# Kernel tuning notes

Measured on AMD Instinct MI355X. Metric: run time of the kernel, lower is better.

## Reference

```python
import jax, jax.numpy as jnp
import numpy as np

N_NODES = 50000
N_EDGES = 1600000
N_GRAPHS = 512
IN_DIM = 64
HID = 128
OUT_DIM = 10


def setup_inputs() -> dict:
    key = jax.random.key(0)
    ks = jax.random.split(key, 12)
    x = jax.random.normal(ks[0], (N_NODES, IN_DIM), dtype=jnp.float32)
    edge_index = jax.random.randint(ks[1], (2, N_EDGES), 0, N_NODES, dtype=jnp.int64)
    batch = jnp.sort(jax.random.randint(ks[2], (N_NODES,), 0, N_GRAPHS, dtype=jnp.int64))
    edge_attr = jax.random.uniform(ks[3], (N_EDGES,), dtype=jnp.float32)
    # glorot-ish init for weights
    def lin(k, fan_in, fan_out):
        s = (6.0 / (fan_in + fan_out)) ** 0.5
        return jax.random.uniform(k, (fan_in, fan_out), minval=-s, maxval=s, dtype=jnp.float32)
    return {
        "x": x, "edge_index": edge_index, "batch": batch, "edge_attr": edge_attr,
        "W1": lin(ks[4], IN_DIM, HID), "b1": jnp.zeros((HID,), jnp.float32),
        "W2": lin(ks[5], HID, HID), "b2": jnp.zeros((HID,), jnp.float32),
        "Wm1": lin(ks[6], HID, HID), "bm1": jnp.zeros((HID,), jnp.float32),
        "Wm2": lin(ks[7], HID, OUT_DIM), "bm2": jnp.zeros((OUT_DIM,), jnp.float32),
    }


def _gcn_conv(x, edge_index, edge_weight, W, b, num_nodes):
    """PyG GCNConv: add self-loops, symmetric norm with edge weights, x@W, scatter-add, +bias."""
    loop = jnp.arange(num_nodes, dtype=edge_index.dtype)
    src = jnp.concatenate([edge_index[0], loop])
    dst = jnp.concatenate([edge_index[1], loop])
    ew = jnp.concatenate([edge_weight, jnp.ones((num_nodes,), edge_weight.dtype)])
    deg = jax.ops.segment_sum(ew, dst, num_segments=num_nodes)  # [N]
    dinv = jnp.where(deg > 0, jax.lax.rsqrt(jnp.where(deg > 0, deg, 1.0)), 0.0)
    norm = dinv[src] * ew * dinv[dst]  # [E+N]
    h = x @ W  # [N, F_out]
    msg = h[src] * norm[:, None]  # gather + scale
    out = jax.ops.segment_sum(msg, dst, num_segments=num_nodes)
    return out + b


def reference(x, edge_index, batch, edge_attr, W1, b1, W2, b2, Wm1, bm1, Wm2, bm2):
    n = x.shape[0]
    h = _gcn_conv(x, edge_index, edge_attr, W1, b1, n)
    h = jax.nn.relu(h)  # dropout = identity in eval mode
    h = _gcn_conv(h, edge_index, edge_attr, W2, b2, n)
    h = jax.nn.relu(h)
    pooled = jax.ops.segment_sum(h, batch, num_segments=N_GRAPHS)  # global_add_pool
    z = jax.nn.relu(pooled @ Wm1 + bm1)
    return z @ Wm2 + bm2  # [num_graphs, out_dim]
```

## Files before the change

kernel.cpp:

```cpp
#include <hip/hip_runtime.h>
#include <hip/hip_bf16.h>
#include <hip/hip_fp16.h>
#include <cstdint>

#define HIDC 128
#define FIXSCALE 4194304.0f
#define FIXINV   (1.0f / 4194304.0f)
#define MAXDEG 80

#define BKT_SHIFT 7
#define BKT_NODES 128
#define BKT_CAP   6144
#define BIN_TILE  4096
#define BIN_THREADS 512

typedef _Float16 half8 __attribute__((ext_vector_type(8)));
typedef float float4v __attribute__((ext_vector_type(4)));

__global__ __launch_bounds__(256) void prep_kernel(
        const float* __restrict__ W1, const float* __restrict__ W2,
        _Float16* __restrict__ W1t, _Float16* __restrict__ W2t,
        unsigned int* __restrict__ tails, int nbkt) {
    int i = blockIdx.x * 256 + threadIdx.x;
    if (i < 16384) { int k = i >> 7, n = i & 127; W2t[n * 128 + k] = (_Float16)W2[i]; }
    if (i < 8192)  { int k = i >> 7, n = i & 127; W1t[n * 64 + k]  = (_Float16)W1[i]; }
    if (i < nbkt) tails[i] = 0u;
}

__global__ __launch_bounds__(BIN_THREADS) void bin_kernel(
        const int* __restrict__ ei, const float* __restrict__ ea,
        unsigned long long* __restrict__ buck, unsigned int* __restrict__ tails,
        int E, int nbkt) {
    __shared__ unsigned long long rec[BIN_TILE];
    __shared__ unsigned int cnt[BIN_THREADS];
    __shared__ unsigned int startx[BIN_THREADS];
    __shared__ unsigned int cur[BIN_THREADS];
    __shared__ unsigned int gbase[BIN_THREADS];
    int t = threadIdx.x;
    int base = blockIdx.x * BIN_TILE;
    int total = E - base; if (total > BIN_TILE) total = BIN_TILE;

    cnt[t] = 0;
    __syncthreads();

    unsigned int lo[8], dv[8];
#pragma unroll
    for (int j = 0; j < 8; ++j) {
        int e = base + j * BIN_THREADS + t;
        if (e < E) {
            int s = ei[e]; int d = ei[E + e]; float w = ea[e];
            lo[j] = (unsigned int)s |
                    ((unsigned int)__half_as_ushort(__float2half_rn(w)) << 16);
            dv[j] = (unsigned int)d;
            atomicAdd(&cnt[dv[j] >> BKT_SHIFT], 1u);
        } else dv[j] = 0xffffffffu;
    }
    __syncthreads();

    startx[t] = cnt[t];
    __syncthreads();
    for (int off = 1; off < BIN_THREADS; off <<= 1) {
        unsigned int add = (t >= off) ? startx[t - off] : 0u;
        __syncthreads();
        startx[t] += add;
        __syncthreads();
    }
    unsigned int excl = startx[t] - cnt[t];
    startx[t] = excl;
    cur[t] = excl;
    if (t < nbkt) gbase[t] = atomicAdd(&tails[t], cnt[t]);
    __syncthreads();

#pragma unroll
    for (int j = 0; j < 8; ++j) {
        if (dv[j] != 0xffffffffu) {
            unsigned int p = atomicAdd(&cur[dv[j] >> BKT_SHIFT], 1u);
            rec[p] = ((unsigned long long)dv[j] << 32) | (unsigned long long)lo[j];
        }
    }
    __syncthreads();

    for (int i = t; i < total; i += BIN_THREADS) {
        unsigned long long r = rec[i];
        unsigned int b = ((unsigned int)(r >> 32)) >> BKT_SHIFT;
        unsigned int idx = gbase[b] + ((unsigned int)i - startx[b]);
        if (idx < BKT_CAP) buck[(size_t)b * BKT_CAP + idx] = r;
    }
}

__global__ __launch_bounds__(256) void fill_kernel(
        const unsigned long long* __restrict__ buck,
        const unsigned int* __restrict__ tails,
        unsigned long long* __restrict__ degcnt,
        unsigned int* __restrict__ padcsr, int n_nodes) {
    __shared__ unsigned long long deg[BKT_NODES];
    int b = blockIdx.x, t = threadIdx.x;
    if (t < BKT_NODES) deg[t] = 0ull;
    __syncthreads();
    int cnt_b = (int)tails[b]; if (cnt_b > BKT_CAP) cnt_b = BKT_CAP;
    const unsigned long long* rb = buck + (size_t)b * BKT_CAP;
    int nodeBase = b << BKT_SHIFT;
    for (int i = t; i < cnt_b; i += 256) {
        unsigned long long r = rb[i];
        unsigned int lo = (unsigned int)r;
        unsigned int dl = ((unsigned int)(r >> 32)) & (BKT_NODES - 1);
        float w = __half2float(__ushort_as_half((unsigned short)(lo >> 16)));
        unsigned int fx = (unsigned int)(w * FIXSCALE + 0.5f);
        unsigned long long old =
            atomicAdd(&deg[dl], (1ull << 32) | (unsigned long long)fx);
        unsigned int rank = (unsigned int)(old >> 32);
        if (rank < MAXDEG)
            padcsr[(size_t)(nodeBase + dl) * MAXDEG + rank] = lo;
    }
    __syncthreads();
    if (t < BKT_NODES) {
        int node = nodeBase + t;
        if (node < n_nodes) degcnt[node] = deg[t];
    }
}

__global__ __launch_bounds__(256) void gemm1_mfma_kernel(
        const float* __restrict__ X,
        const _Float16* __restrict__ W1t,
        const unsigned long long* __restrict__ degcnt,
        __half* __restrict__ out, int n_nodes) {
    int wave = threadIdx.x >> 6, lane = threadIdx.x & 63;
    int nodeBase = (blockIdx.x * 4 + wave) * 16;
    if (nodeBase >= n_nodes) return;
    int mrow = lane & 15, quad = lane >> 4;

    int anode = nodeBase + mrow; if (anode >= n_nodes) anode = n_nodes - 1;
    const float* Arow = X + (size_t)anode * 64 + quad * 8;
    half8 a[2];
#pragma unroll
    for (int q = 0; q < 2; ++q) {
        float4v f0 = *(const float4v*)(Arow + q * 32);
        float4v f1 = *(const float4v*)(Arow + q * 32 + 4);
        half8 hv;
#pragma unroll
        for (int j = 0; j < 4; ++j) { hv[j] = (_Float16)f0[j]; hv[j + 4] = (_Float16)f1[j]; }
        a[q] = hv;
    }

    float4v acc[8];
#pragma unroll
    for (int nt = 0; nt < 8; ++nt) acc[nt] = (float4v)(0.f);
#pragma unroll
    for (int nt = 0; nt < 8; ++nt) {
        const _Float16* Brow = W1t + (size_t)(nt * 16 + mrow) * 64 + quad * 8;
#pragma unroll
        for (int q = 0; q < 2; ++q) {
            half8 b = *(const half8*)(Brow + q * 32);
            acc[nt] = __builtin_amdgcn_mfma_f32_16x16x32_f16(a[q], b, acc[nt], 0, 0, 0);
        }
    }
#pragma unroll
    for (int r = 0; r < 4; ++r) {
        int node = nodeBase + quad * 4 + r;
        if (node < n_nodes) {
            unsigned long long v = degcnt[node];
            float di = rsqrtf(1.0f + (float)(unsigned int)(v & 0xffffffffull) * FIXINV);
#pragma unroll
            for (int nt = 0; nt < 8; ++nt)
                out[(size_t)node * 128 + nt * 16 + mrow] = __float2half(acc[nt][r] * di);
        }
    }
}

__global__ __launch_bounds__(256) void gemm2_mfma_kernel(
        const __half* __restrict__ A,
        const _Float16* __restrict__ W2t,
        const unsigned long long* __restrict__ degcnt,
        __half* __restrict__ out, int n_nodes) {
    int wave = threadIdx.x >> 6, lane = threadIdx.x & 63;
    int nodeBase = (blockIdx.x * 4 + wave) * 16;
    if (nodeBase >= n_nodes) return;
    int mrow = lane & 15, quad = lane >> 4;

    int anode = nodeBase + mrow; if (anode >= n_nodes) anode = n_nodes - 1;
    const _Float16* Arow = (const _Float16*)A + (size_t)anode * 128 + quad * 8;
    half8 a[4];
#pragma unroll
    for (int q = 0; q < 4; ++q) a[q] = *(const half8*)(Arow + q * 32);

    float4v acc[8];
#pragma unroll
    for (int nt = 0; nt < 8; ++nt) acc[nt] = (float4v)(0.f);
#pragma unroll
    for (int nt = 0; nt < 8; ++nt) {
        const _Float16* Brow = W2t + (size_t)(nt * 16 + mrow) * 128 + quad * 8;
#pragma unroll
        for (int q = 0; q < 4; ++q) {
            half8 b = *(const half8*)(Brow + q * 32);
            acc[nt] = __builtin_amdgcn_mfma_f32_16x16x32_f16(a[q], b, acc[nt], 0, 0, 0);
        }
    }
#pragma unroll
    for (int r = 0; r < 4; ++r) {
        int node = nodeBase + quad * 4 + r;
        if (node < n_nodes) {
            unsigned long long v = degcnt[node];
            float di = rsqrtf(1.0f + (float)(unsigned int)(v & 0xffffffffull) * FIXINV);
#pragma unroll
            for (int nt = 0; nt < 8; ++nt)
                out[(size_t)node * 128 + nt * 16 + mrow] = __float2half(acc[nt][r] * di);
        }
    }
}

__global__ __launch_bounds__(256) void agg_kernel(const __half* __restrict__ h,
                                                  const unsigned long long* __restrict__ degcnt,
                                                  const unsigned int* __restrict__ padcsr,
                                                  const float* __restrict__ bias,
                                                  __half* __restrict__ out, int n_nodes) {
    int wave = threadIdx.x >> 6;
    int lane = threadIdx.x & 63;
    int node = blockIdx.x * 4 + wave;
    if (node >= n_nodes) return;
    unsigned long long v = degcnt[node];
    int cnt = (int)(v >> 32);
    if (cnt > MAXDEG) cnt = MAXDEG;
    float di = rsqrtf(1.0f + (float)(unsigned int)(v & 0xffffffffull) * FIXINV);
    const unsigned int* row = padcsr + (size_t)node * MAXDEG;
    float a0 = 0.f, a1 = 0.f;
    int e = 0;
    for (; e + 16 <= cnt; e += 16) {
        unsigned int p[16];
#pragma unroll
        for (int j = 0; j < 16; ++j) p[j] = row[e + j];
        __half2 vv[16];
#pragma unroll
        for (int j = 0; j < 16; ++j)
            vv[j] = *(reinterpret_cast<const __half2*>(h + (p[j] & 0xffffu) * HIDC) + lane);
#pragma unroll
        for (int j = 0; j < 16; ++j) {
            float c = __half2float(__ushort_as_half((unsigned short)(p[j] >> 16)));
            float2 f = __half22float2(vv[j]);
            a0 = fmaf(c, f.x, a0); a1 = fmaf(c, f.y, a1);
        }
    }
    for (; e + 4 <= cnt; e += 4) {
        unsigned int p[4];
#pragma unroll
        for (int j = 0; j < 4; ++j) p[j] = row[e + j];
        __half2 vv[4];
#pragma unroll
        for (int j = 0; j < 4; ++j)
            vv[j] = *(reinterpret_cast<const __half2*>(h + (p[j] & 0xffffu) * HIDC) + lane);
#pragma unroll
        for (int j = 0; j < 4; ++j) {
            float c = __half2float(__ushort_as_half((unsigned short)(p[j] >> 16)));
            float2 f = __half22float2(vv[j]);
            a0 = fmaf(c, f.x, a0); a1 = fmaf(c, f.y, a1);
        }
    }
    for (; e < cnt; ++e) {
        unsigned int p = row[e];
        float c = __half2float(__ushort_as_half((unsigned short)(p >> 16)));
        float2 f = __half22float2(*(reinterpret_cast<const __half2*>(h + (p & 0xffffu) * HIDC) + lane));
        a0 = fmaf(c, f.x, a0); a1 = fmaf(c, f.y, a1);
    }
    float2 fn = __half22float2(*(reinterpret_cast<const __half2*>(h + (size_t)node * HIDC) + lane));
    a0 = di * (a0 + fn.x);
    a1 = di * (a1 + fn.y);
    float2 bb = *(reinterpret_cast<const float2*>(bias) + lane);
    a0 = fmaxf(a0 + bb.x, 0.f);
    a1 = fmaxf(a1 + bb.y, 0.f);
    *(reinterpret_cast<__half2*>(out + (size_t)node * HIDC) + lane) =
        __floats2half2_rn(a0, a1);
}

__global__ __launch_bounds__(128) void pool_mlp_kernel(const __half* __restrict__ h,
                                                       const int* __restrict__ batch,
                                                       const float* __restrict__ Wm1,
                                                       const float* __restrict__ bm1,
                                                       const float* __restrict__ Wm2,
                                                       const float* __restrict__ bm2,
                                                       float* __restrict__ out,
                                                       int n_nodes, int out_dim) {
    int g = blockIdx.x;
    int t = threadIdx.x;
    __shared__ int sb[2];
    if (t < 2) {
        int target = g + t;
        int lo = 0, hi = n_nodes;
        while (lo < hi) { int mid = (lo + hi) >> 1; if (batch[mid] < target) lo = mid + 1; else hi = mid; }
        sb[t] = lo;
    }
    __syncthreads();
    int beg = sb[0], end = sb[1];
    float p = 0.f;
    for (int i = beg; i < end; ++i) p += __half2float(h[(size_t)i * 128 + t]);
    __shared__ float row[128];
    __shared__ float z[128];
    row[t] = p;
    __syncthreads();
    float acc = bm1[t];
#pragma unroll 8
    for (int k = 0; k < 128; ++k) acc += row[k] * Wm1[k * 128 + t];
    z[t] = fmaxf(acc, 0.f);
    __syncthreads();
    if (t < out_dim) {
        float o = bm2[t];
#pragma unroll 8
        for (int k = 0; k < 128; ++k) o += z[k] * Wm2[k * out_dim + t];
        out[g * out_dim + t] = o;
    }
}

extern "C" void kernel_launch(void* const* d_in, const int* in_sizes, int n_in,
                              void* d_out, int out_size, void* d_ws, size_t ws_size,
                              hipStream_t stream) {
    const float* x   = (const float*)d_in[0];
    const int*   ei  = (const int*)d_in[1];
    const int*   bat = (const int*)d_in[2];
    const float* ea  = (const float*)d_in[3];
    const float* W1  = (const float*)d_in[4];
    const float* b1  = (const float*)d_in[5];
    const float* W2  = (const float*)d_in[6];
    const float* b2  = (const float*)d_in[7];
    const float* Wm1 = (const float*)d_in[8];
    const float* bm1 = (const float*)d_in[9];
    const float* Wm2 = (const float*)d_in[10];
    const float* bm2 = (const float*)d_in[11];
    float* out = (float*)d_out;

    const int N = in_sizes[2];
    const int E = in_sizes[1] / 2;
    const int N_GRAPHS = 512;
    const int OUT_DIM = out_size / N_GRAPHS;

    char* ws = (char*)d_ws;
    size_t off = 0;
    auto alloc = [&](size_t bytes) { char* p = ws + off; off += (bytes + 255) & ~size_t(255); return p; };
    __half* bufA    = (__half*)alloc((size_t)N * HIDC * 2);
    __half* bufR    = (__half*)alloc((size_t)N * HIDC * 2);
    unsigned int* padcsr = (unsigned int*)alloc((size_t)N * MAXDEG * 4);
    unsigned long long* degcnt = (unsigned long long*)alloc((size_t)N * 8);
    _Float16* W2t   = (_Float16*)alloc(128 * 128 * 2);
    _Float16* W1t   = (_Float16*)alloc(128 * 64 * 2);
    unsigned int* tails = (unsigned int*)alloc(BIN_THREADS * 4);

    unsigned long long* buck = (unsigned long long*)bufA;
    int nbkt = (N + BKT_NODES - 1) >> BKT_SHIFT;

    prep_kernel<<<64, 256, 0, stream>>>(W1, W2, W1t, W2t, tails, nbkt);
    int binBlocks = (E + BIN_TILE - 1) / BIN_TILE;
    bin_kernel<<<binBlocks, BIN_THREADS, 0, stream>>>(ei, ea, buck, tails, E, nbkt);
    fill_kernel<<<nbkt, 256, 0, stream>>>(buck, tails, degcnt, padcsr, N);
    gemm1_mfma_kernel<<<(N + 63) / 64, 256, 0, stream>>>(x, W1t, degcnt, bufA, N);
    agg_kernel<<<(N + 3) / 4, 256, 0, stream>>>(bufA, degcnt, padcsr, b1, bufR, N);
    gemm2_mfma_kernel<<<(N + 63) / 64, 256, 0, stream>>>(bufR, W2t, degcnt, bufA, N);
    agg_kernel<<<(N + 3) / 4, 256, 0, stream>>>(bufA, degcnt, padcsr, b2, bufR, N);
    pool_mlp_kernel<<<N_GRAPHS, 128, 0, stream>>>(bufR, bat, Wm1, bm1, Wm2, bm2, out, N, OUT_DIM);
}
```

Before: 303.4 us.

## Reorder GCN layers to aggregate before transform and shrink bucket records

Layer 1 now aggregates the 64-wide pre-scaled input features (computed in fill_kernel) before the GEMM, and layer 2 aggregates before multiplying by W2. Bias and ReLU are folded into the GEMM epilogues. The first aggregation gathers half as much data, and the second GEMM no longer needs the degree scaling. Bucket records are split into a 4-byte payload plus a 1-byte local destination with a smaller capacity, the bin scan uses wave shuffles, and the pool kernel uses 256 threads. The risks are fp16 rounding in a different order and possible bucket overflow at the reduced capacity.

New measurement: 278.3 us. -8.3%, faster.

```diff
diff --git a/kernel.cpp b/kernel.cpp
--- a/kernel.cpp
+++ b/kernel.cpp
@@ -10,7 +10,7 @@
 
 #define BKT_SHIFT 7
 #define BKT_NODES 128
-#define BKT_CAP   6144
+#define BKT_CAP   4608
 #define BIN_TILE  4096
 #define BIN_THREADS 512
 
@@ -29,13 +29,14 @@
 
 __global__ __launch_bounds__(BIN_THREADS) void bin_kernel(
         const int* __restrict__ ei, const float* __restrict__ ea,
-        unsigned long long* __restrict__ buck, unsigned int* __restrict__ tails,
-        int E, int nbkt) {
+        unsigned int* __restrict__ buck_lo, unsigned char* __restrict__ buck_dl,
+        unsigned int* __restrict__ tails, int E, int nbkt) {
     __shared__ unsigned long long rec[BIN_TILE];
     __shared__ unsigned int cnt[BIN_THREADS];
     __shared__ unsigned int startx[BIN_THREADS];
     __shared__ unsigned int cur[BIN_THREADS];
     __shared__ unsigned int gbase[BIN_THREADS];
+    __shared__ unsigned int wtot[BIN_THREADS / 64];
     int t = threadIdx.x;
     int base = blockIdx.x * BIN_TILE;
     int total = E - base; if (total > BIN_TILE) total = BIN_TILE;
@@ -57,18 +58,22 @@
     }
     __syncthreads();
 
-    startx[t] = cnt[t];
-    __syncthreads();
-    for (int off = 1; off < BIN_THREADS; off <<= 1) {
-        unsigned int add = (t >= off) ? startx[t - off] : 0u;
-        __syncthreads();
-        startx[t] += add;
-        __syncthreads();
-    }
-    unsigned int excl = startx[t] - cnt[t];
+    unsigned int c = cnt[t];
+    unsigned int sc = c;
+#pragma unroll
+    for (int off = 1; off < 64; off <<= 1) {
+        unsigned int v = __shfl_up(sc, off);
+        if ((t & 63) >= off) sc += v;
+    }
+    if ((t & 63) == 63) wtot[t >> 6] = sc;
+    __syncthreads();
+    unsigned int wbase = 0;
+    int w = t >> 6;
+    for (int i = 0; i < w; ++i) wbase += wtot[i];
+    unsigned int excl = sc + wbase - c;
     startx[t] = excl;
     cur[t] = excl;
-    if (t < nbkt) gbase[t] = atomicAdd(&tails[t], cnt[t]);
+    if (t < nbkt) gbase[t] = atomicAdd(&tails[t], c);
     __syncthreads();
 
 #pragma unroll
@@ -82,28 +87,35 @@
 
     for (int i = t; i < total; i += BIN_THREADS) {
         unsigned long long r = rec[i];
-        unsigned int b = ((unsigned int)(r >> 32)) >> BKT_SHIFT;
+        unsigned int hi = (unsigned int)(r >> 32);
+        unsigned int b = hi >> BKT_SHIFT;
         unsigned int idx = gbase[b] + ((unsigned int)i - startx[b]);
-        if (idx < BKT_CAP) buck[(size_t)b * BKT_CAP + idx] = r;
+        if (idx < BKT_CAP) {
+            buck_lo[b * BKT_CAP + idx] = (unsigned int)r;
+            buck_dl[b * BKT_CAP + idx] = (unsigned char)(hi & (BKT_NODES - 1));
+        }
     }
 }
 
 __global__ __launch_bounds__(256) void fill_kernel(
-        const unsigned long long* __restrict__ buck,
+        const unsigned int* __restrict__ buck_lo,
+        const unsigned char* __restrict__ buck_dl,
         const unsigned int* __restrict__ tails,
+        const float* __restrict__ x,
         unsigned long long* __restrict__ degcnt,
-        unsigned int* __restrict__ padcsr, int n_nodes) {
+        unsigned int* __restrict__ padcsr,
+        _Float16* __restrict__ xt, int n_nodes) {
     __shared__ unsigned long long deg[BKT_NODES];
+    __shared__ float sdinv[BKT_NODES];
     int b = blockIdx.x, t = threadIdx.x;
     if (t < BKT_NODES) deg[t] = 0ull;
     __syncthreads();
     int cnt_b = (int)tails[b]; if (cnt_b > BKT_CAP) cnt_b = BKT_CAP;
-    const unsigned long long* rb = buck + (size_t)b * BKT_CAP;
+    unsigned int boff = (unsigned int)b * BKT_CAP;
     int nodeBase = b << BKT_SHIFT;
     for (int i = t; i < cnt_b; i += 256) {
-        unsigned long long r = rb[i];
-        unsigned int lo = (unsigned int)r;
-        unsigned int dl = ((unsigned int)(r >> 32)) & (BKT_NODES - 1);
+        unsigned int lo = buck_lo[boff + i];
+        unsigned int dl = buck_dl[boff + i];
         float w = __half2float(__ushort_as_half((unsigned short)(lo >> 16)));
         unsigned int fx = (unsigned int)(w * FIXSCALE + 0.5f);
         unsigned long long old =
@@ -114,14 +126,85 @@
     }
     __syncthreads();
     if (t < BKT_NODES) {
+        unsigned long long dv = deg[t];
+        sdinv[t] = rsqrtf(1.0f + (float)(unsigned int)(dv & 0xffffffffull) * FIXINV);
         int node = nodeBase + t;
-        if (node < n_nodes) degcnt[node] = deg[t];
-    }
+        if (node < n_nodes) degcnt[node] = dv;
+    }
+    __syncthreads();
+    int d = t & 63, nl = t >> 6;
+    for (int nn = nl; nn < BKT_NODES; nn += 4) {
+        int node = nodeBase + nn;
+        if (node < n_nodes)
+            xt[(size_t)node * 64 + d] = (_Float16)(x[(size_t)node * 64 + d] * sdinv[nn]);
+    }
+}
+
+__global__ __launch_bounds__(256) void agg0_kernel(
+        const _Float16* __restrict__ xt,
+        const unsigned long long* __restrict__ degcnt,
+        const unsigned int* __restrict__ padcsr,
+        _Float16* __restrict__ g, int n_nodes) {
+    int wave = threadIdx.x >> 6, lane = threadIdx.x & 63;
+    int node = blockIdx.x * 4 + wave;
+    if (node >= n_nodes) return;
+    int half = lane >> 5, li = lane & 31;
+    unsigned long long v = degcnt[node];
+    int cnt = (int)(v >> 32); if (cnt > MAXDEG) cnt = MAXDEG;
+    float di = rsqrtf(1.0f + (float)(unsigned int)(v & 0xffffffffull) * FIXINV);
+    const unsigned int* row = padcsr + (size_t)node * MAXDEG;
+    const __half2* X = (const __half2*)xt;
+    float a0 = 0.f, a1 = 0.f;
+    int e = 0;
+    for (; e + 32 <= cnt; e += 32) {
+        unsigned int p[16];
+#pragma unroll
+        for (int j = 0; j < 16; ++j) p[j] = row[e + 2 * j + half];
+        __half2 vv[16];
+#pragma unroll
+        for (int j = 0; j < 16; ++j)
+            vv[j] = X[(p[j] & 0xffffu) * 32u + (unsigned)li];
+#pragma unroll
+        for (int j = 0; j < 16; ++j) {
+            float c = __half2float(__ushort_as_half((unsigned short)(p[j] >> 16)));
+            float2 f = __half22float2(vv[j]);
+            a0 = fmaf(c, f.x, a0); a1 = fmaf(c, f.y, a1);
+        }
+    }
+    if (e < cnt) {
+        int rem = cnt - e;
+        unsigned int p[16]; bool m[16];
+#pragma unroll
+        for (int j = 0; j < 16; ++j) {
+            int idx = 2 * j + half;
+            m[j] = idx < rem;
+            p[j] = m[j] ? row[e + idx] : 0u;
+        }
+        __half2 vv[16];
+#pragma unroll
+        for (int j = 0; j < 16; ++j)
+            vv[j] = X[(p[j] & 0xffffu) * 32u + (unsigned)li];
+#pragma unroll
+        for (int j = 0; j < 16; ++j) {
+            float c = m[j] ? __half2float(__ushort_as_half((unsigned short)(p[j] >> 16))) : 0.f;
+            float2 f = __half22float2(vv[j]);
+            a0 = fmaf(c, f.x, a0); a1 = fmaf(c, f.y, a1);
+        }
+    }
+    if (half == 0) {
+        float2 f = __half22float2(X[(unsigned)node * 32u + (unsigned)li]);
+        a0 += f.x; a1 += f.y;
+    }
+    a0 += __shfl_xor(a0, 32);
+    a1 += __shfl_xor(a1, 32);
+    if (half == 0)
+        *((__half2*)g + (unsigned)node * 32u + li) = __floats2half2_rn(di * a0, di * a1);
 }
 
 __global__ __launch_bounds__(256) void gemm1_mfma_kernel(
-        const float* __restrict__ X,
+        const _Float16* __restrict__ G,
         const _Float16* __restrict__ W1t,
+        const float* __restrict__ b1,
         const unsigned long long* __restrict__ degcnt,
         __half* __restrict__ out, int n_nodes) {
     int wave = threadIdx.x >> 6, lane = threadIdx.x & 63;
@@ -130,17 +213,10 @@
     int mrow = lane & 15, quad = lane >> 4;
 
     int anode = nodeBase + mrow; if (anode >= n_nodes) anode = n_nodes - 1;
-    const float* Arow = X + (size_t)anode * 64 + quad * 8;
+    const _Float16* Arow = G + (size_t)anode * 64 + quad * 8;
     half8 a[2];
-#pragma unroll
-    for (int q = 0; q < 2; ++q) {
-        float4v f0 = *(const float4v*)(Arow + q * 32);
-        float4v f1 = *(const float4v*)(Arow + q * 32 + 4);
-        half8 hv;
-#pragma unroll
-        for (int j = 0; j < 4; ++j) { hv[j] = (_Float16)f0[j]; hv[j + 4] = (_Float16)f1[j]; }
-        a[q] = hv;
-    }
+    a[0] = *(const half8*)(Arow);
+    a[1] = *(const half8*)(Arow + 32);
 
     float4v acc[8];
 #pragma unroll
@@ -161,58 +237,19 @@
             unsigned long long v = degcnt[node];
             float di = rsqrtf(1.0f + (float)(unsigned int)(v & 0xffffffffull) * FIXINV);
 #pragma unroll
-            for (int nt = 0; nt < 8; ++nt)
-                out[(size_t)node * 128 + nt * 16 + mrow] = __float2half(acc[nt][r] * di);
-        }
-    }
-}
-
-__global__ __launch_bounds__(256) void gemm2_mfma_kernel(
-        const __half* __restrict__ A,
-        const _Float16* __restrict__ W2t,
-        const unsigned long long* __restrict__ degcnt,
-        __half* __restrict__ out, int n_nodes) {
-    int wave = threadIdx.x >> 6, lane = threadIdx.x & 63;
-    int nodeBase = (blockIdx.x * 4 + wave) * 16;
-    if (nodeBase >= n_nodes) return;
-    int mrow = lane & 15, quad = lane >> 4;
-
-    int anode = nodeBase + mrow; if (anode >= n_nodes) anode = n_nodes - 1;
-    const _Float16* Arow = (const _Float16*)A + (size_t)anode * 128 + quad * 8;
-    half8 a[4];
-#pragma unroll
-    for (int q = 0; q < 4; ++q) a[q] = *(const half8*)(Arow + q * 32);
-
-    float4v acc[8];
-#pragma unroll
-    for (int nt = 0; nt < 8; ++nt) acc[nt] = (float4v)(0.f);
-#pragma unroll
-    for (int nt = 0; nt < 8; ++nt) {
-        const _Float16* Brow = W2t + (size_t)(nt * 16 + mrow) * 128 + quad * 8;
-#pragma unroll
-        for (int q = 0; q < 4; ++q) {
-            half8 b = *(const half8*)(Brow + q * 32);
-            acc[nt] = __builtin_amdgcn_mfma_f32_16x16x32_f16(a[q], b, acc[nt], 0, 0, 0);
-        }
-    }
-#pragma unroll
-    for (int r = 0; r < 4; ++r) {
-        int node = nodeBase + quad * 4 + r;
-        if (node < n_nodes) {
-            unsigned long long v = degcnt[node];
-            float di = rsqrtf(1.0f + (float)(unsigned int)(v & 0xffffffffull) * FIXINV);
-#pragma unroll
-            for (int nt = 0; nt < 8; ++nt)
-                out[(size_t)node * 128 + nt * 16 + mrow] = __float2half(acc[nt][r] * di);
-        }
-    }
-}
-
-__global__ __launch_bounds__(256) void agg_kernel(const __half* __restrict__ h,
-                                                  const unsigned long long* __restrict__ degcnt,
-                                                  const unsigned int* __restrict__ padcsr,
-                                                  const float* __restrict__ bias,
-                                                  __half* __restrict__ out, int n_nodes) {
+            for (int nt = 0; nt < 8; ++nt) {
+                int col = nt * 16 + mrow;
+                float val = fmaxf(acc[nt][r] + b1[col], 0.f) * di;
+                out[(size_t)node * 128 + col] = __float2half(val);
+            }
+        }
+    }
+}
+
+__global__ __launch_bounds__(256) void agg2_kernel(const __half* __restrict__ h,
+                                                   const unsigned long long* __restrict__ degcnt,
+                                                   const unsigned int* __restrict__ padcsr,
+                                                   __half* __restrict__ out, int n_nodes) {
     int wave = threadIdx.x >> 6;
     int lane = threadIdx.x & 63;
     int node = blockIdx.x * 4 + wave;
@@ -263,14 +300,53 @@
     float2 fn = __half22float2(*(reinterpret_cast<const __half2*>(h + (size_t)node * HIDC) + lane));
     a0 = di * (a0 + fn.x);
     a1 = di * (a1 + fn.y);
-    float2 bb = *(reinterpret_cast<const float2*>(bias) + lane);
-    a0 = fmaxf(a0 + bb.x, 0.f);
-    a1 = fmaxf(a1 + bb.y, 0.f);
     *(reinterpret_cast<__half2*>(out + (size_t)node * HIDC) + lane) =
         __floats2half2_rn(a0, a1);
 }
 
-__global__ __launch_bounds__(128) void pool_mlp_kernel(const __half* __restrict__ h,
+__global__ __launch_bounds__(256) void gemm2_mfma_kernel(
+        const __half* __restrict__ A,
+        const _Float16* __restrict__ W2t,
+        const float* __restrict__ b2,
+        __half* __restrict__ out, int n_nodes) {
+    int wave = threadIdx.x >> 6, lane = threadIdx.x & 63;
+    int nodeBase = (blockIdx.x * 4 + wave) * 16;
+    if (nodeBase >= n_nodes) return;
+    int mrow = lane & 15, quad = lane >> 4;
+
+    int anode = nodeBase + mrow; if (anode >= n_nodes) anode = n_nodes - 1;
+    const _Float16* Arow = (const _Float16*)A + (size_t)anode * 128 + quad * 8;
+    half8 a[4];
+#pragma unroll
+    for (int q = 0; q < 4; ++q) a[q] = *(const half8*)(Arow + q * 32);
+
+    float4v acc[8];
+#pragma unroll
+    for (int nt = 0; nt < 8; ++nt) acc[nt] = (float4v)(0.f);
+#pragma unroll
+    for (int nt = 0; nt < 8; ++nt) {
+        const _Float16* Brow = W2t + (size_t)(nt * 16 + mrow) * 128 + quad * 8;
+#pragma unroll
+        for (int q = 0; q < 4; ++q) {
+            half8 b = *(const half8*)(Brow + q * 32);
+            acc[nt] = __builtin_amdgcn_mfma_f32_16x16x32_f16(a[q], b, acc[nt], 0, 0, 0);
+        }
+    }
+#pragma unroll
+    for (int r = 0; r < 4; ++r) {
+        int node = nodeBase + quad * 4 + r;
+        if (node < n_nodes) {
+#pragma unroll
+            for (int nt = 0; nt < 8; ++nt) {
+                int col = nt * 16 + mrow;
+                float val = fmaxf(acc[nt][r] + b2[col], 0.f);
+                out[(size_t)node * 128 + col] = __float2half(val);
+            }
+        }
+    }
+}
+
+__global__ __launch_bounds__(256) void pool_mlp_kernel(const __half* __restrict__ h,
                                                        const int* __restrict__ batch,
                                                        const float* __restrict__ Wm1,
                                                        const float* __restrict__ bm1,
@@ -281,6 +357,9 @@
     int g = blockIdx.x;
     int t = threadIdx.x;
     __shared__ int sb[2];
+    __shared__ float row2[256];
+    __shared__ float row[128];
+    __shared__ float zl[128];
     if (t < 2) {
         int target = g + t;
         int lo = 0, hi = n_nodes;
@@ -289,21 +368,25 @@
     }
     __syncthreads();
     int beg = sb[0], end = sb[1];
+    int dim = t & 127, sub = t >> 7;
     float p = 0.f;
-    for (int i = beg; i < end; ++i) p += __half2float(h[(size_t)i * 128 + t]);
-    __shared__ float row[128];
-    __shared__ float z[128];
-    row[t] = p;
-    __syncthreads();
-    float acc = bm1[t];
+    for (int i = beg + sub; i < end; i += 2)
+        p += __half2float(h[(size_t)i * 128 + dim]);
+    row2[t] = p;
+    __syncthreads();
+    if (t < 128) row[t] = row2[t] + row2[t + 128];
+    __syncthreads();
+    if (t < 128) {
+        float acc = bm1[t];
 #pragma unroll 8
-    for (int k = 0; k < 128; ++k) acc += row[k] * Wm1[k * 128 + t];
-    z[t] = fmaxf(acc, 0.f);
+        for (int k = 0; k < 128; ++k) acc += row[k] * Wm1[k * 128 + t];
+        zl[t] = fmaxf(acc, 0.f);
+    }
     __syncthreads();
     if (t < out_dim) {
         float o = bm2[t];
 #pragma unroll 8
-        for (int k = 0; k < 128; ++k) o += z[k] * Wm2[k * out_dim + t];
+        for (int k = 0; k < 128; ++k) o += zl[k] * Wm2[k * out_dim + t];
         out[g * out_dim + t] = o;
     }
 }
@@ -333,24 +416,31 @@
     char* ws = (char*)d_ws;
     size_t off = 0;
     auto alloc = [&](size_t bytes) { char* p = ws + off; off += (bytes + 255) & ~size_t(255); return p; };
-    __half* bufA    = (__half*)alloc((size_t)N * HIDC * 2);
-    __half* bufR    = (__half*)alloc((size_t)N * HIDC * 2);
-    unsigned int* padcsr = (unsigned int*)alloc((size_t)N * MAXDEG * 4);
+    char* regB = alloc((size_t)N * HIDC * 2);
+    char* regC = alloc((size_t)N * HIDC * 2);
+    char* regA = alloc((size_t)N * MAXDEG * 4);
     unsigned long long* degcnt = (unsigned long long*)alloc((size_t)N * 8);
-    _Float16* W2t   = (_Float16*)alloc(128 * 128 * 2);
-    _Float16* W1t   = (_Float16*)alloc(128 * 64 * 2);
+    _Float16* W2t = (_Float16*)alloc(128 * 128 * 2);
+    _Float16* W1t = (_Float16*)alloc(128 * 64 * 2);
     unsigned int* tails = (unsigned int*)alloc(BIN_THREADS * 4);
 
-    unsigned long long* buck = (unsigned long long*)bufA;
     int nbkt = (N + BKT_NODES - 1) >> BKT_SHIFT;
+    unsigned int*  buck_lo = (unsigned int*)regB;
+    unsigned char* buck_dl = (unsigned char*)(regB + (size_t)nbkt * BKT_CAP * 4);
+    __half*    htld = (__half*)regB;
+    _Float16*  xt   = (_Float16*)regC;
+    _Float16*  gbuf = (_Float16*)(regC + (size_t)N * 64 * 2);
+    __half*    ubuf = (__half*)regC;
+    unsigned int* padcsr = (unsigned int*)regA;
+    __half*    zbuf = (__half*)regA;
 
     prep_kernel<<<64, 256, 0, stream>>>(W1, W2, W1t, W2t, tails, nbkt);
     int binBlocks = (E + BIN_TILE - 1) / BIN_TILE;
-    bin_kernel<<<binBlocks, BIN_THREADS, 0, stream>>>(ei, ea, buck, tails, E, nbkt);
-    fill_kernel<<<nbkt, 256, 0, stream>>>(buck, tails, degcnt, padcsr, N);
-    gemm1_mfma_kernel<<<(N + 63) / 64, 256, 0, stream>>>(x, W1t, degcnt, bufA, N);
-    agg_kernel<<<(N + 3) / 4, 256, 0, stream>>>(bufA, degcnt, padcsr, b1, bufR, N);
-    gemm2_mfma_kernel<<<(N + 63) / 64, 256, 0, stream>>>(bufR, W2t, degcnt, bufA, N);
-    agg_kernel<<<(N + 3) / 4, 256, 0, stream>>>(bufA, degcnt, padcsr, b2, bufR, N);
-    pool_mlp_kernel<<<N_GRAPHS, 128, 0, stream>>>(bufR, bat, Wm1, bm1, Wm2, bm2, out, N, OUT_DIM);
-}
+    bin_kernel<<<binBlocks, BIN_THREADS, 0, stream>>>(ei, ea, buck_lo, buck_dl, tails, E, nbkt);
+    fill_kernel<<<nbkt, 256, 0, stream>>>(buck_lo, buck_dl, tails, x, degcnt, padcsr, xt, N);
+    agg0_kernel<<<(N + 3) / 4, 256, 0, stream>>>(xt, degcnt, padcsr, gbuf, N);
+    gemm1_mfma_kernel<<<(N + 63) / 64, 256, 0, stream>>>(gbuf, W1t, b1, degcnt, htld, N);
+    agg2_kernel<<<(N + 3) / 4, 256, 0, stream>>>(htld, degcnt, padcsr, ubuf, N);
+    gemm2_mfma_kernel<<<(N + 63) / 64, 256, 0, stream>>>(ubuf, W2t, b2, zbuf, N);
+    pool_mlp_kernel<<<N_GRAPHS, 256, 0, stream>>>(zbuf, bat, Wm1, bm1, Wm2, bm2, out, N, OUT_DIM);
+}
```
